# Kernel optimization log

Measured on AMD Instinct MI355X. Metric: run time of the kernel, lower is better.

## Reference

```python
import jax, jax.numpy as jnp
import numpy as np
import math

B, T, N, C = 1, 12, 10000, 32
TIME_DIM, N_SUP, E, NODE_EMB = 8, 3, 320000, 32
S = N_SUP + 2  # support_len + 2 slots after concat


def setup_inputs() -> dict:
    key = jax.random.key(0)
    ks = jax.random.split(key, 16)
    inp = {
        'x': jax.random.normal(ks[0], (B, T, N, C), jnp.float32),
        'timeoh': jax.random.uniform(ks[1], (B, 43), jnp.float32),
        'edges': jax.random.randint(ks[2], (N_SUP, 2, E), 0, N),
        # shared dy_gat params (attention_list reuses the same ModuleList)
        'mlp_w': jax.random.normal(ks[3], (C, C), jnp.float32) * 0.05,
        'mlp_b': jnp.zeros((C,), jnp.float32),
        'temb_w': jax.random.normal(ks[4], (43, TIME_DIM), jnp.float32) * 0.1,
        'atten_pool': jax.random.normal(ks[5], (TIME_DIM, 2 * C), jnp.float32) * 0.1,
        # adaptive-adjacency gcn branch
        'node2vec': jax.random.normal(ks[6], (N, NODE_EMB), jnp.float32) * 0.1,
        'gcn_w': jax.random.normal(ks[7], (3 * C, C), jnp.float32) * 0.05,
        'gcn_b': jnp.zeros((C,), jnp.float32),
        # slot self-attention over S supports
        'q_w': jax.random.normal(ks[8], (C, 6 * C), jnp.float32) * 0.05,
        'q_b': jnp.zeros((6 * C,), jnp.float32),
        'k_w': jax.random.normal(ks[9], (C, 6 * C), jnp.float32) * 0.05,
        'k_b': jnp.zeros((6 * C,), jnp.float32),
        'v_w': jax.random.normal(ks[10], (C, 6 * C), jnp.float32) * 0.05,
        'v_b': jnp.zeros((6 * C,), jnp.float32),
        'dense_w': jax.random.normal(ks[11], (6 * C, C), jnp.float32) * 0.05,
        'dense_b': jnp.zeros((C,), jnp.float32),
    }
    return inp


def _dy_gat(x, timeoh, src, dst, mlp_w, mlp_b, temb_w, atten_pool):
    h = x @ mlp_w + mlp_b                                   # (B,T,N,C)
    attn = (timeoh @ temb_w) @ atten_pool                    # (B,2C)
    # einsum('btnc,bc->btn') over concatenated [h_src, h_dst] splits additively
    s_src = jnp.einsum('btnc,bc->btn', h, attn[:, :C])
    s_dst = jnp.einsum('btnc,bc->btn', h, attn[:, C:])
    values = s_src[:, :, src] + s_dst[:, :, dst]             # (B,T,E)
    p = jax.nn.leaky_relu(values, 0.01)
    e = jnp.exp(p - jnp.max(p, axis=2, keepdims=True))       # global (per b,t) max-shift
    rowsum = jnp.zeros((B, T, N), e.dtype).at[:, :, src].add(e)
    h_prime = jnp.zeros_like(h).at[:, :, src].add(e[..., None] * h[:, :, dst, :])
    h_prime = h_prime / (rowsum[..., None] + 9e-15)
    return jax.nn.elu(h_prime)  # concat=True


def reference(x, timeoh, edges, mlp_w, mlp_b, temb_w, atten_pool,
              node2vec, gcn_w, gcn_b, q_w, q_b, k_w, k_b, v_w, v_b,
              dense_w, dense_b):
    outs = [x]
    for i in range(N_SUP):
        outs.append(_dy_gat(x, timeoh, edges[i, 0], edges[i, 1],
                            mlp_w, mlp_b, temb_w, atten_pool))
    # adaptive graph conv (static, order=2, support_len=1)
    adj = jax.nn.softmax(jax.nn.relu(node2vec @ node2vec.T), axis=1)  # (N,N)
    x1 = jnp.einsum('wv,btvf->btwf', adj, x)
    x2 = jnp.einsum('wv,btvf->btwf', adj, x1)
    x_adp = jnp.concatenate([x, x1, x2], -1) @ gcn_w + gcn_b
    outs.append(x_adp)
    out = jnp.concatenate(outs, -1).reshape(B, T, N, S, C)
    q = out @ q_w + q_b                                       # (B,T,N,S,6C)
    k = out @ k_w + k_b
    v = out @ v_w + v_b
    scores = jnp.einsum('btnsd,btnud->btnsu', q, k) / math.sqrt(6 * C)
    a = jax.nn.softmax(scores, axis=-1)
    o = jnp.einsum('btnsu,btnud->btnsd', a, v)
    o = o @ dense_w + dense_b                                 # (B,T,N,S,C)
    return jax.nn.elu(jnp.mean(o, axis=-2))                   # (B,T,N,C)
```

## Files before the change

### kernel.cpp

```cpp
#include <hip/hip_runtime.h>
#include <hip/hip_bf16.h>

#define T_ 12
#define N_ 10000
#define C_ 32
#define E_ 320000
#define SUP_ 3
#define TN_ (T_*N_)

typedef __attribute__((ext_vector_type(4))) float f32x4;
typedef __attribute__((ext_vector_type(8))) short bf16x8;
typedef __attribute__((ext_vector_type(4))) short bf16x4;

__device__ __forceinline__ short bf16c(float f) {
  __hip_bfloat16 b = __float2bfloat16(f);
  return (short)__builtin_bit_cast(unsigned short, b);
}

#if __has_builtin(__builtin_amdgcn_exp2f)
#define EXP2F(x) __builtin_amdgcn_exp2f(x)
#else
#define EXP2F(x) exp2f(x)
#endif

#define PRM_ATTN 0
#define PRM_G    64
#define PRM_H    1088
#define PRM_G1   2112
#define PRM_G2   2144
#define PRM_HB   2176
#define PRM_G0   2208

__global__ __launch_bounds__(256) void k_prep(
    const float* __restrict__ timeoh, const float* __restrict__ temb_w,
    const float* __restrict__ atten_pool,
    const float* __restrict__ q_w, const float* __restrict__ q_b,
    const float* __restrict__ k_w, const float* __restrict__ k_b,
    const float* __restrict__ v_w, const float* __restrict__ v_b,
    const float* __restrict__ dense_w, const float* __restrict__ dense_b,
    float* __restrict__ prm) {
  __shared__ float tv[8];
  int tid = threadIdx.x;
  if (tid < 8) {
    float s = 0.f;
    for (int j = 0; j < 43; j++) s += timeoh[j] * temb_w[j * 8 + tid];
    tv[tid] = s;
  }
  __syncthreads();
  if (tid < 64) {
    float s = 0.f;
    for (int d = 0; d < 8; d++) s += tv[d] * atten_pool[d * 64 + tid];
    prm[PRM_ATTN + tid] = s;
  }
  for (int idx = tid; idx < 1024; idx += 256) {
    int r = idx >> 5, c = idx & 31;
    float s = 0.f, s2 = 0.f;
    for (int d = 0; d < 192; d++) {
      s  += q_w[r * 192 + d] * k_w[c * 192 + d];
      s2 += v_w[r * 192 + d] * dense_w[d * 32 + c];
    }
    prm[PRM_G + idx] = s;
    prm[PRM_H + idx] = s2;
  }
  if (tid < 32) {
    float s = 0.f, s2 = 0.f, s3 = 0.f;
    for (int d = 0; d < 192; d++) {
      s  += q_w[tid * 192 + d] * k_b[d];
      s2 += k_w[tid * 192 + d] * q_b[d];
      s3 += v_b[d] * dense_w[d * 32 + tid];
    }
    prm[PRM_G1 + tid] = s;
    prm[PRM_G2 + tid] = s2;
    prm[PRM_HB + tid] = s3 + dense_b[tid];
  }
  if (tid == 0) {
    float s = 0.f;
    for (int d = 0; d < 192; d++) s += q_b[d] * k_b[d];
    prm[PRM_G0] = s;
  }
}

__global__ __launch_bounds__(256) void k_h(
    const float* __restrict__ x, const float* __restrict__ mlp_w,
    const float* __restrict__ mlp_b, const float* __restrict__ prm,
    __hip_bfloat16* __restrict__ h16, float* __restrict__ s_src,
    float* __restrict__ s_dst) {
  __shared__ float W[32 * 32];
  __shared__ float bsh[32], attnsh[64];
  __shared__ float xs[8][32];
  int tid = threadIdx.x;
  for (int i = tid; i < 1024; i += 256) W[i] = mlp_w[i];
  if (tid < 32) bsh[tid] = mlp_b[tid];
  if (tid < 64) attnsh[tid] = prm[PRM_ATTN + tid];
  long base = (long)blockIdx.x * 8;
  int nloc = tid >> 5, c = tid & 31;
  long row = base + nloc;
  xs[nloc][c] = x[row * 32 + c];
  __syncthreads();
  float hval = bsh[c];
#pragma unroll
  for (int k = 0; k < 32; k++) hval = fmaf(xs[nloc][k], W[k * 32 + c], hval);
  h16[row * 32 + c] = __float2bfloat16(hval);
  float a = hval * attnsh[c], b = hval * attnsh[32 + c];
#pragma unroll
  for (int m = 16; m >= 1; m >>= 1) {
    a += __shfl_xor(a, m, 64);
    b += __shfl_xor(b, m, 64);
  }
  if (c == 0) { s_src[row] = a; s_dst[row] = b; }
}

__global__ __launch_bounds__(256) void k_hist(const int* __restrict__ edges,
                                              int* __restrict__ cnt) {
  int sup = blockIdx.y;
  int e = blockIdx.x * 256 + threadIdx.x;
  const int* src = edges + (long)sup * 2 * E_;
  atomicAdd(&cnt[sup * N_ + src[e]], 1);
}

__global__ __launch_bounds__(1024) void k_scan(const int* __restrict__ cnt,
                                               int* __restrict__ offs,
                                               int* __restrict__ cur) {
  __shared__ int sh[1024];
  __shared__ int run;
  int sup = blockIdx.x, tid = threadIdx.x;
  if (tid == 0) run = 0;
  __syncthreads();
  for (int base = 0; base < N_; base += 1024) {
    int i = base + tid;
    int v = (i < N_) ? cnt[sup * N_ + i] : 0;
    sh[tid] = v;
    __syncthreads();
    for (int off = 1; off < 1024; off <<= 1) {
      int t = (tid >= off) ? sh[tid - off] : 0;
      __syncthreads();
      sh[tid] += t;
      __syncthreads();
    }
    int runv = run;
    int excl = runv + sh[tid] - v;
    if (i < N_) {
      offs[sup * (N_ + 1) + i] = excl;
      cur[sup * N_ + i] = excl;
    }
    __syncthreads();
    if (tid == 0) run = runv + sh[1023];
    __syncthreads();
  }
  if (tid == 0) offs[sup * (N_ + 1) + N_] = run;
}

__global__ __launch_bounds__(256) void k_fill(const int* __restrict__ edges,
                                              int* __restrict__ cur,
                                              int* __restrict__ csr) {
  int sup = blockIdx.y;
  int e = blockIdx.x * 256 + threadIdx.x;
  const int* src = edges + (long)sup * 2 * E_;
  const int* dst = src + E_;
  int pos = atomicAdd(&cur[sup * N_ + src[e]], 1);
  csr[sup * E_ + pos] = dst[e];
}

__global__ __launch_bounds__(256) void k_max(const int* __restrict__ edges,
                                             const float* __restrict__ s_src,
                                             const float* __restrict__ s_dst,
                                             unsigned* __restrict__ menc) {
  int sup = blockIdx.z, t = blockIdx.y;
  const int* src = edges + (long)sup * 2 * E_;
  const int* dst = src + E_;
  const float* ss = s_src + (long)t * N_;
  const float* sd = s_dst + (long)t * N_;
  float m = -1e30f;
  int lim = (blockIdx.x + 1) * 10000;
  for (int e = blockIdx.x * 10000 + threadIdx.x; e < lim; e += 256) {
    float v = ss[src[e]] + sd[dst[e]];
    v = (v >= 0.f) ? v : 0.01f * v;
    m = fmaxf(m, v);
  }
#pragma unroll
  for (int k = 32; k >= 1; k >>= 1) m = fmaxf(m, __shfl_xor(m, k, 64));
  if ((threadIdx.x & 63) == 0) {
    unsigned bits = __float_as_uint(m);
    unsigned enc = (bits & 0x80000000u) ? ~bits : (bits | 0x80000000u);
    atomicMax(&menc[sup * T_ + t], enc);
  }
}

__global__ __launch_bounds__(256) void k_gather(
    const int* __restrict__ csr, const int* __restrict__ offs,
    const float* __restrict__ s_src, const float* __restrict__ s_dst,
    const unsigned* __restrict__ menc, const __hip_bfloat16* __restrict__ h16,
    __hip_bfloat16* __restrict__ hp16) {
  const int sup = blockIdx.z, t = blockIdx.y;
  const int wave = threadIdx.x >> 6, lane = threadIdx.x & 63;
  const int n = blockIdx.x * 4 + wave;
  unsigned enc = menc[sup * T_ + t];
  unsigned mb = (enc & 0x80000000u) ? (enc & 0x7fffffffu) : ~enc;
  const float M = __uint_as_float(mb);
  const float a = s_src[(long)t * N_ + n];
  const int off = offs[sup * (N_ + 1) + n], end = offs[sup * (N_ + 1) + n + 1];
  const float* sd = s_dst + (long)t * N_;
  const uint4* hb4 = (const uint4*)(h16 + (long)t * N_ * 32);
  const int* csrs = csr + sup * E_;
  const int slot = lane >> 2, cl = lane & 3;
  const int clamp = (end > off) ? (end - 1) : 0;

  float acc[8];
#pragma unroll
  for (int j = 0; j < 8; j++) acc[j] = 0.f;
  float psum = 0.f;

  const int idx0 = off + slot;
  int d0 = csrs[min(idx0, clamp)];
  int d1 = csrs[min(idx0 + 16, clamp)];
  float sd0 = sd[d0];
  uint4 u0 = hb4[d0 * 4 + cl];

  for (int idx = idx0; idx < end; idx += 16) {
    int d2 = csrs[min(idx + 32, clamp)];
    float sd1 = sd[d1];
    uint4 u1 = hb4[d1 * 4 + cl];
    float v = a + sd0;
    v = fmaxf(v, 0.01f * v);
    float p = __expf(v - M);
    psum += p;
    acc[0] = fmaf(p, __uint_as_float(u0.x << 16),        acc[0]);
    acc[1] = fmaf(p, __uint_as_float(u0.x & 0xffff0000u), acc[1]);
    acc[2] = fmaf(p, __uint_as_float(u0.y << 16),        acc[2]);
    acc[3] = fmaf(p, __uint_as_float(u0.y & 0xffff0000u), acc[3]);
    acc[4] = fmaf(p, __uint_as_float(u0.z << 16),        acc[4]);
    acc[5] = fmaf(p, __uint_as_float(u0.z & 0xffff0000u), acc[5]);
    acc[6] = fmaf(p, __uint_as_float(u0.w << 16),        acc[6]);
    acc[7] = fmaf(p, __uint_as_float(u0.w & 0xffff0000u), acc[7]);
    d1 = d2; sd0 = sd1; u0 = u1;
  }

#pragma unroll
  for (int m = 4; m <= 32; m <<= 1) psum += __shfl_xor(psum, m, 64);
#pragma unroll
  for (int j = 0; j < 8; j++) {
#pragma unroll
    for (int m = 4; m <= 32; m <<= 1) acc[j] += __shfl_xor(acc[j], m, 64);
  }

  if (slot == 0) {
    float inv = 1.f / (psum + 9e-15f);
    unsigned w[4];
#pragma unroll
    for (int q = 0; q < 4; q++) {
      float h0 = acc[2 * q + 0] * inv;
      float h1 = acc[2 * q + 1] * inv;
      h0 = (h0 > 0.f) ? h0 : (__expf(h0) - 1.f);
      h1 = (h1 > 0.f) ? h1 : (__expf(h1) - 1.f);
      unsigned lo = (unsigned)(unsigned short)__builtin_bit_cast(unsigned short, __float2bfloat16(h0));
      unsigned hi = (unsigned)(unsigned short)__builtin_bit_cast(unsigned short, __float2bfloat16(h1));
      w[q] = lo | (hi << 16);
    }
    ((uint4*)hp16)[((long)sup * TN_ + (long)t * N_ + n) * 4 + cl] = uint4{w[0], w[1], w[2], w[3]};
  }
}

__global__ __launch_bounds__(256) void k_n2vA(const float* __restrict__ n2v,
                                              short* __restrict__ n2vA) {
  const float SC = 1.2011224087864498f;
  int idx = blockIdx.x * 256 + threadIdx.x;
  if (idx >= N_ * 4) return;
  int row = idx >> 2, l4 = idx & 3;
  short v[8];
#pragma unroll
  for (int h = 0; h < 2; h++)
#pragma unroll
    for (int j = 0; j < 4; j++)
      v[h * 4 + j] = bf16c(n2v[row * 32 + 16 * h + 4 * l4 + j] * SC);
  *(bf16x8*)&n2vA[(long)idx * 8] = bf16x8{v[0], v[1], v[2], v[3], v[4], v[5], v[6], v[7]};
}

template <int WITHR>
__global__ __launch_bounds__(256) void k_pack(const float* __restrict__ src,
                                              const float* __restrict__ rinv,
                                              short* __restrict__ xq) {
  int idx = blockIdx.x * 256 + threadIdx.x;
  int ck = idx / 1536;
  int rem = idx - ck * 1536;
  int l4 = rem / 384;
  int col = rem - l4 * 384;
  int t = col >> 5, f = col & 31;
  const long cb = (long)t * N_ * 32 + f;
  short v[8];
#pragma unroll
  for (int e = 0; e < 8; e++) {
    int vv = ck * 32 + 4 * l4 + (e & 3) + 16 * (e >> 2);
    float a = 0.f;
    if (vv < N_) {
      a = src[cb + (long)vv * 32];
      if (WITHR) a *= rinv[vv];
    }
    v[e] = bf16c(a);
  }
  *(bf16x8*)&xq[(long)idx * 8] = bf16x8{v[0], v[1], v[2], v[3], v[4], v[5], v[6], v[7]};
}

template <int PASS>
__global__ __launch_bounds__(512, 2) void k_adj12(const short* __restrict__ n2vA,
                                                  const short* __restrict__ xq,
                                                  float* __restrict__ out,
                                                  float* __restrict__ Rout) {
  __shared__ __align__(16) short aPl[2][8 * 4 * 64 * 8];
  const int tid = threadIdx.x;
  const int lane = tid & 63;
  const int wv = tid >> 6;
  const int l15 = lane & 15;
  const int l4 = lane >> 4;
  const int brow0 = blockIdx.x * 64;
  const int colbase = wv * 48;

  bf16x8 bw[4];
#pragma unroll
  for (int mt = 0; mt < 4; mt++) {
    int row = brow0 + mt * 16 + l15;
    row = row < N_ ? row : N_ - 1;
    bw[mt] = *(const bf16x8*)&n2vA[((long)row * 4 + l4) * 8];
  }

  f32x4 acc[4][3];
#pragma unroll
  for (int i = 0; i < 4; i++)
#pragma unroll
    for (int j = 0; j < 3; j++) acc[i][j] = f32x4{0.f, 0.f, 0.f, 0.f};
  float racc[4] = {0.f, 0.f, 0.f, 0.f};

#define PHASE_A(cexpr, slab)                                                              \
  {                                                                                       \
    const int c_ = (cexpr);                                                               \
    if (c_ < 313) {                                                                       \
      const int vb_ = c_ * 32;                                                            \
      int r1_ = vb_ + 16 + l15; r1_ = r1_ < N_ ? r1_ : N_ - 1;                            \
      bf16x8 av0_ = *(const bf16x8*)&n2vA[((long)(vb_ + l15) * 4 + l4) * 8];              \
      bf16x8 av1_ = *(const bf16x8*)&n2vA[((long)r1_ * 4 + l4) * 8];                      \
      _Pragma("unroll")                                                                   \
      for (int mt = 0; mt < 4; mt++) {                                                    \
        f32x4 s0_ = __builtin_amdgcn_mfma_f32_16x16x32_bf16(av0_, bw[mt],                 \
                                                            f32x4{0.f,0.f,0.f,0.f},0,0,0);\
        f32x4 s1_ = __builtin_amdgcn_mfma_f32_16x16x32_bf16(av1_, bw[mt],                 \
                                                            f32x4{0.f,0.f,0.f,0.f},0,0,0);\
        short pp_[8];                                                                     \
        float rs0_ = 0.f, rs1_ = 0.f;                                                     \
        _Pragma("unroll")                                                                 \
        for (int j = 0; j < 4; j++) {                                                     \
          float p0_ = EXP2F(fmaxf(s0_[j], 0.f));                                          \
          float p1_ = EXP2F(fmaxf(s1_[j], 0.f));                                          \
          if constexpr (PASS == 1) { rs0_ += p0_; rs1_ += p1_; }                          \
          pp_[j] = bf16c(p0_);                                                            \
          pp_[j + 4] = bf16c(p1_);                                                        \
        }                                                                                 \
        *(bf16x8*)&aPl[slab][((wv * 4 + mt) * 64 + lane) * 8] =                           \
            bf16x8{pp_[0],pp_[1],pp_[2],pp_[3],pp_[4],pp_[5],pp_[6],pp_[7]};              \
        if constexpr (PASS == 1) racc[mt] += (c_ != 312) ? (rs0_ + rs1_) : rs0_;          \
      }                                                                                   \
    }                                                                                     \
  }

  PHASE_A(wv, 0)
  __syncthreads();

  for (int g = 0; g < 40; g++) {
    const int cur = g & 1;
    if (g + 1 < 40) PHASE_A((g + 1) * 8 + wv, cur ^ 1)

    const int rem = 313 - g * 8;
    if (rem >= 8) {
      bf16x8 bx[24];
#pragma unroll
      for (int cc = 0; cc < 8; cc++) {
        const long xb = (long)(g * 8 + cc) * 1536 + (long)l4 * 384;
        bx[cc * 3 + 0] = *(const bf16x8*)&xq[(xb + colbase + 0 * 16 + l15) * 8];
        bx[cc * 3 + 1] = *(const bf16x8*)&xq[(xb + colbase + 1 * 16 + l15) * 8];
        bx[cc * 3 + 2] = *(const bf16x8*)&xq[(xb + colbase + 2 * 16 + l15) * 8];
      }
#pragma unroll
      for (int cc = 0; cc < 8; cc++) {
#pragma unroll
        for (int mt = 0; mt < 4; mt++) {
          bf16x8 aP = *(const bf16x8*)&aPl[cur][((cc * 4 + mt) * 64 + lane) * 8];
          acc[mt][0] = __builtin_amdgcn_mfma_f32_16x16x32_bf16(aP, bx[cc * 3 + 0], acc[mt][0], 0, 0, 0);
          acc[mt][1] = __builtin_amdgcn_mfma_f32_16x16x32_bf16(aP, bx[cc * 3 + 1], acc[mt][1], 0, 0, 0);
          acc[mt][2] = __builtin_amdgcn_mfma_f32_16x16x32_bf16(aP, bx[cc * 3 + 2], acc[mt][2], 0, 0, 0);
        }
      }
    } else {
      for (int cc = 0; cc < rem; cc++) {
        const long xb = (long)(g * 8 + cc) * 1536 + (long)l4 * 384;
        bf16x8 bx0 = *(const bf16x8*)&xq[(xb + colbase + 0 * 16 + l15) * 8];
        bf16x8 bx1 = *(const bf16x8*)&xq[(xb + colbase + 1 * 16 + l15) * 8];
        bf16x8 bx2 = *(const bf16x8*)&xq[(xb + colbase + 2 * 16 + l15) * 8];
#pragma unroll
        for (int mt = 0; mt < 4; mt++) {
          bf16x8 aP = *(const bf16x8*)&aPl[cur][((cc * 4 + mt) * 64 + lane) * 8];
          acc[mt][0] = __builtin_amdgcn_mfma_f32_16x16x32_bf16(aP, bx0, acc[mt][0], 0, 0, 0);
          acc[mt][1] = __builtin_amdgcn_mfma_f32_16x16x32_bf16(aP, bx1, acc[mt][1], 0, 0, 0);
          acc[mt][2] = __builtin_amdgcn_mfma_f32_16x16x32_bf16(aP, bx2, acc[mt][2], 0, 0, 0);
        }
      }
    }
    __syncthreads();
  }
#undef PHASE_A

  if constexpr (PASS == 1) {
#pragma unroll
    for (int mt = 0; mt < 4; mt++) {
      float r = racc[mt];
      r += __shfl_xor(r, 16, 64);
      r += __shfl_xor(r, 32, 64);
      int w = brow0 + mt * 16 + l15;
      if (l4 == 0 && w < N_) atomicAdd(&Rout[w], r);
    }
  }
#pragma unroll
  for (int mt = 0; mt < 4; mt++) {
#pragma unroll
    for (int nt = 0; nt < 3; nt++) {
      const int col = colbase + nt * 16 + l15;
      const int t = col >> 5, f = col & 31;
#pragma unroll
      for (int j = 0; j < 4; j++) {
        const int w = brow0 + mt * 16 + 4 * l4 + j;
        if (w < N_) out[((long)t * N_ + w) * 32 + f] = acc[mt][nt][j];
      }
    }
  }
}

__global__ __launch_bounds__(256) void k_rinv(float* __restrict__ R) {
  int i = blockIdx.x * 256 + threadIdx.x;
  if (i < N_) R[i] = 1.f / R[i];
}

__global__ __launch_bounds__(256) void k_gcn(const float* __restrict__ x,
                                             const float* __restrict__ x1,
                                             float* __restrict__ x2io,
                                             const float* __restrict__ Rinv,
                                             const float* __restrict__ gcn_w,
                                             const float* __restrict__ gcn_b) {
  __shared__ float W[96 * 32];
  __shared__ float bsh[32];
  __shared__ float rows[8][96];
  int tid = threadIdx.x;
  for (int i = tid; i < 96 * 32; i += 256) W[i] = gcn_w[i];
  if (tid < 32) bsh[tid] = gcn_b[tid];
  long base = (long)blockIdx.x * 8;
  int nloc = tid >> 5, c = tid & 31;
  long row = base + nloc;
  long nIdx = row % N_;
  float ri = Rinv[nIdx];
  rows[nloc][c] = x[row * 32 + c];
  rows[nloc][32 + c] = x1[row * 32 + c] * ri;
  rows[nloc][64 + c] = x2io[row * 32 + c] * ri;
  __syncthreads();
  float o = bsh[c];
#pragma unroll
  for (int k = 0; k < 96; k++) o = fmaf(rows[nloc][k], W[k * 32 + c], o);
  __syncthreads();
  x2io[row * 32 + c] = o;
}

__device__ __forceinline__ void load_row(int s, long r, const float* __restrict__ x,
                                         const __hip_bfloat16* __restrict__ hp16,
                                         const float* __restrict__ xadp, float* m) {
  if (s == 0 || s == 4) {
    const float4* p = (const float4*)((s == 0 ? x : xadp) + r * 32);
#pragma unroll
    for (int q = 0; q < 8; q++) {
      float4 v = p[q];
      m[q * 4 + 0] = v.x; m[q * 4 + 1] = v.y; m[q * 4 + 2] = v.z; m[q * 4 + 3] = v.w;
    }
  } else {
    const uint4* p = (const uint4*)(hp16 + ((long)(s - 1) * TN_ + r) * 32);
#pragma unroll
    for (int q = 0; q < 4; q++) {
      uint4 v = p[q];
      unsigned uu[4] = {v.x, v.y, v.z, v.w};
#pragma unroll
      for (int j = 0; j < 4; j++) {
        m[q * 8 + j * 2 + 0] = __uint_as_float(uu[j] << 16);
        m[q * 8 + j * 2 + 1] = __uint_as_float(uu[j] & 0xffff0000u);
      }
    }
  }
}

__global__ __launch_bounds__(256) void k_attn(const float* __restrict__ x,
                                              const __hip_bfloat16* __restrict__ hp16,
                                              const float* __restrict__ xadp,
                                              const float* __restrict__ prm,
                                              float* __restrict__ out) {
  __shared__ float Gs[1024], Hs[1024], g1s[32], g2s[32], hbs[32];
  __shared__ float g0sh;
  int tid = threadIdx.x;
  for (int i = tid; i < 1024; i += 256) { Gs[i] = prm[PRM_G + i]; Hs[i] = prm[PRM_H + i]; }
  if (tid < 32) { g1s[tid] = prm[PRM_G1 + tid]; g2s[tid] = prm[PRM_G2 + tid]; hbs[tid] = prm[PRM_HB + tid]; }
  if (tid == 0) g0sh = prm[PRM_G0];
  __syncthreads();
  long r = (long)blockIdx.x * 256 + tid;
  if (r >= TN_) return;
  float g0 = g0sh;
  float sc[5][5], d1[5], d2[5];
  float ms[32], mu[32], y[32];
#pragma unroll
  for (int s = 0; s < 5; s++) {
    load_row(s, r, x, hp16, xadp, ms);
    float a = 0.f, b = 0.f;
#pragma unroll
    for (int k = 0; k < 32; k++) { a = fmaf(ms[k], g1s[k], a); b = fmaf(ms[k], g2s[k], b); }
    d1[s] = a; d2[s] = b;
#pragma unroll
    for (int c = 0; c < 32; c++) {
      float s2 = 0.f;
#pragma unroll
      for (int k = 0; k < 32; k++) s2 = fmaf(ms[k], Gs[k * 32 + c], s2);
      y[c] = s2;
    }
#pragma unroll
    for (int u = 0; u < 5; u++) {
      load_row(u, r, x, hp16, xadp, mu);
      float dt = 0.f;
#pragma unroll
      for (int k = 0; k < 32; k++) dt = fmaf(y[k], mu[k], dt);
      sc[s][u] = dt;
    }
  }
  const float rs = 0.07216878364870322f;
  float abar[5];
#pragma unroll
  for (int u = 0; u < 5; u++) abar[u] = 0.f;
#pragma unroll
  for (int s = 0; s < 5; s++) {
    float e[5];
    float mx = -1e30f;
#pragma unroll
    for (int u = 0; u < 5; u++) {
      float v = (sc[s][u] + d1[s] + d2[u] + g0) * rs;
      e[u] = v;
      mx = fmaxf(mx, v);
    }
    float sm = 0.f;
#pragma unroll
    for (int u = 0; u < 5; u++) { e[u] = __expf(e[u] - mx); sm += e[u]; }
    float inv = 1.f / sm;
#pragma unroll
    for (int u = 0; u < 5; u++) abar[u] = fmaf(e[u], inv, abar[u]);
  }
  float z[32];
#pragma unroll
  for (int k = 0; k < 32; k++) z[k] = 0.f;
#pragma unroll
  for (int u = 0; u < 5; u++) {
    load_row(u, r, x, hp16, xadp, mu);
    float w = abar[u] * 0.2f;
#pragma unroll
    for (int k = 0; k < 32; k++) z[k] = fmaf(w, mu[k], z[k]);
  }
#pragma unroll
  for (int c = 0; c < 32; c++) {
    float o = hbs[c];
#pragma unroll
    for (int k = 0; k < 32; k++) o = fmaf(z[k], Hs[k * 32 + c], o);
    o = (o > 0.f) ? o : (__expf(o) - 1.f);
    out[r * 32 + c] = o;
  }
}

extern "C" void kernel_launch(void* const* d_in, const int* in_sizes, int n_in,
                              void* d_out, int out_size, void* d_ws, size_t ws_size,
                              hipStream_t stream) {
  (void)in_sizes; (void)n_in; (void)out_size; (void)ws_size;
  const float* x          = (const float*)d_in[0];
  const float* timeoh     = (const float*)d_in[1];
  const int*   edges      = (const int*)d_in[2];
  const float* mlp_w      = (const float*)d_in[3];
  const float* mlp_b      = (const float*)d_in[4];
  const float* temb_w     = (const float*)d_in[5];
  const float* atten_pool = (const float*)d_in[6];
  const float* node2vec   = (const float*)d_in[7];
  const float* gcn_w      = (const float*)d_in[8];
  const float* gcn_b      = (const float*)d_in[9];
  const float* q_w  = (const float*)d_in[10];
  const float* q_b  = (const float*)d_in[11];
  const float* k_w  = (const float*)d_in[12];
  const float* k_b  = (const float*)d_in[13];
  const float* v_w  = (const float*)d_in[14];
  const float* v_b  = (const float*)d_in[15];
  const float* dense_w = (const float*)d_in[16];
  const float* dense_b = (const float*)d_in[17];
  float* out = (float*)d_out;
  char* ws = (char*)d_ws;

  float*    prm  = (float*)(ws + 0);
  unsigned* menc = (unsigned*)(ws + 9216);
  int*      cnt  = (int*)(ws + 9472);
  int*      cur  = (int*)(ws + 129472);
  int*      offs = (int*)(ws + 249472);
  float*    ssrc = (float*)(ws + 369664);
  float*    sdst = (float*)(ws + 849664);
  float*    R    = (float*)(ws + 1329664);
  __hip_bfloat16* h16  = (__hip_bfloat16*)(ws + 1369664);
  int*      csr  = (int*)(ws + 9049664);
  __hip_bfloat16* hp16 = (__hip_bfloat16*)(ws + 12889664);
  float*    x1   = (float*)(ws + 35929664);
  float*    x2   = (float*)(ws + 51289664);
  short*    n2vA = (short*)(ws + 66649664);
  short*    xq0  = (short*)(ws + 67289664);
  short*    xq1  = (short*)(ws + 74983488);

  (void)hipMemsetAsync(menc, 0, 144, stream);
  (void)hipMemsetAsync(cnt, 0, 120000, stream);
  (void)hipMemsetAsync(R, 0, 40000, stream);

  k_prep<<<1, 256, 0, stream>>>(timeoh, temb_w, atten_pool, q_w, q_b, k_w, k_b,
                                v_w, v_b, dense_w, dense_b, prm);
  k_h<<<15000, 256, 0, stream>>>(x, mlp_w, mlp_b, prm, h16, ssrc, sdst);
  k_hist<<<dim3(1250, 3), 256, 0, stream>>>(edges, cnt);
  k_scan<<<3, 1024, 0, stream>>>(cnt, offs, cur);
  k_fill<<<dim3(1250, 3), 256, 0, stream>>>(edges, cur, csr);
  k_max<<<dim3(32, 12, 3), 256, 0, stream>>>(edges, ssrc, sdst, menc);
  k_gather<<<dim3(2500, 12, 3), 256, 0, stream>>>(csr, offs, ssrc, sdst, menc, h16, hp16);

  k_n2vA<<<157, 256, 0, stream>>>(node2vec, n2vA);
  k_pack<0><<<1878, 256, 0, stream>>>(x, nullptr, xq0);
  k_adj12<1><<<157, 512, 0, stream>>>(n2vA, xq0, x1, R);
  k_rinv<<<40, 256, 0, stream>>>(R);
  k_pack<1><<<1878, 256, 0, stream>>>(x1, R, xq1);
  k_adj12<2><<<157, 512, 0, stream>>>(n2vA, xq1, x2, nullptr);
  k_gcn<<<15000, 256, 0, stream>>>(x, x1, x2, R, gcn_w, gcn_b);
  k_attn<<<469, 256, 0, stream>>>(x, hp16, x2, prm, out);
}
```

Measured before the change: 923.8 us.

## Retile adjacency GEMM to 128 rows by 192 columns per block

The fused adjacency-softmax-times-x kernel now gives each block 128 output rows and half of the 384 columns, on a 79x2 grid instead of 157 blocks. The 8 waves split both the exp(score) tile generation (two row halves by four column chunks) and the MFMA accumulation (two row groups by four column groups). Each block now produces a larger probability tile per stage and reuses it across more rows, so less score recomputation happens per output. In exchange, the exp work is duplicated across the two column-half blocks, and the row-sum atomics are restricted to blockIdx.y==0.

```diff
diff --git a/kernel.cpp b/kernel.cpp
--- a/kernel.cpp
+++ b/kernel.cpp
@@ -301,23 +301,27 @@
 }
 
 template <int PASS>
-__global__ __launch_bounds__(512, 2) void k_adj12(const short* __restrict__ n2vA,
+__global__ __launch_bounds__(512, 2) void k_adj13(const short* __restrict__ n2vA,
                                                   const short* __restrict__ xq,
                                                   float* __restrict__ out,
                                                   float* __restrict__ Rout) {
-  __shared__ __align__(16) short aPl[2][8 * 4 * 64 * 8];
+  __shared__ __align__(16) short aPl[2][4 * 8 * 64 * 8];
   const int tid = threadIdx.x;
   const int lane = tid & 63;
   const int wv = tid >> 6;
   const int l15 = lane & 15;
   const int l4 = lane >> 4;
-  const int brow0 = blockIdx.x * 64;
-  const int colbase = wv * 48;
+  const int brow0 = blockIdx.x * 128;
+  const int mh = wv & 1;
+  const int cslot = wv >> 1;
+  const int mgrp = wv >> 2;
+  const int cgw = wv & 3;
+  const int colg = blockIdx.y * 192 + cgw * 48;
 
   bf16x8 bw[4];
 #pragma unroll
   for (int mt = 0; mt < 4; mt++) {
-    int row = brow0 + mt * 16 + l15;
+    int row = brow0 + (mh * 4 + mt) * 16 + l15;
     row = row < N_ ? row : N_ - 1;
     bw[mt] = *(const bf16x8*)&n2vA[((long)row * 4 + l4) * 8];
   }
@@ -329,11 +333,11 @@
     for (int j = 0; j < 3; j++) acc[i][j] = f32x4{0.f, 0.f, 0.f, 0.f};
   float racc[4] = {0.f, 0.f, 0.f, 0.f};
 
-#define PHASE_A(cexpr, slab)                                                              \
+#define PHASE_A(gexpr, slab)                                                              \
   {                                                                                       \
-    const int c_ = (cexpr);                                                               \
-    if (c_ < 313) {                                                                       \
-      const int vb_ = c_ * 32;                                                            \
+    const int co_ = (gexpr) * 4 + cslot;                                                  \
+    if (co_ < 313) {                                                                      \
+      const int vb_ = co_ * 32;                                                           \
       int r1_ = vb_ + 16 + l15; r1_ = r1_ < N_ ? r1_ : N_ - 1;                            \
       bf16x8 av0_ = *(const bf16x8*)&n2vA[((long)(vb_ + l15) * 4 + l4) * 8];              \
       bf16x8 av1_ = *(const bf16x8*)&n2vA[((long)r1_ * 4 + l4) * 8];                      \
@@ -353,49 +357,50 @@
           pp_[j] = bf16c(p0_);                                                            \
           pp_[j + 4] = bf16c(p1_);                                                        \
         }                                                                                 \
-        *(bf16x8*)&aPl[slab][((wv * 4 + mt) * 64 + lane) * 8] =                           \
+        *(bf16x8*)&aPl[slab][((cslot * 8 + mh * 4 + mt) * 64 + lane) * 8] =               \
             bf16x8{pp_[0],pp_[1],pp_[2],pp_[3],pp_[4],pp_[5],pp_[6],pp_[7]};              \
-        if constexpr (PASS == 1) racc[mt] += (c_ != 312) ? (rs0_ + rs1_) : rs0_;          \
+        if constexpr (PASS == 1) racc[mt] += (co_ != 312) ? (rs0_ + rs1_) : rs0_;         \
       }                                                                                   \
     }                                                                                     \
   }
 
-  PHASE_A(wv, 0)
+  PHASE_A(0, 0)
   __syncthreads();
 
-  for (int g = 0; g < 40; g++) {
+  const int NGRP = 79;
+  for (int g = 0; g < NGRP; g++) {
     const int cur = g & 1;
-    if (g + 1 < 40) PHASE_A((g + 1) * 8 + wv, cur ^ 1)
-
-    const int rem = 313 - g * 8;
-    if (rem >= 8) {
-      bf16x8 bx[24];
-#pragma unroll
-      for (int cc = 0; cc < 8; cc++) {
-        const long xb = (long)(g * 8 + cc) * 1536 + (long)l4 * 384;
-        bx[cc * 3 + 0] = *(const bf16x8*)&xq[(xb + colbase + 0 * 16 + l15) * 8];
-        bx[cc * 3 + 1] = *(const bf16x8*)&xq[(xb + colbase + 1 * 16 + l15) * 8];
-        bx[cc * 3 + 2] = *(const bf16x8*)&xq[(xb + colbase + 2 * 16 + l15) * 8];
+    if (g + 1 < NGRP) PHASE_A(g + 1, cur ^ 1)
+
+    const int rem0 = 313 - g * 4;
+    if (rem0 >= 4) {
+      bf16x8 bx[12];
+#pragma unroll
+      for (int cc = 0; cc < 4; cc++) {
+        const long xb = (long)(g * 4 + cc) * 1536 + (long)l4 * 384;
+        bx[cc * 3 + 0] = *(const bf16x8*)&xq[(xb + colg + 0 * 16 + l15) * 8];
+        bx[cc * 3 + 1] = *(const bf16x8*)&xq[(xb + colg + 1 * 16 + l15) * 8];
+        bx[cc * 3 + 2] = *(const bf16x8*)&xq[(xb + colg + 2 * 16 + l15) * 8];
       }
 #pragma unroll
-      for (int cc = 0; cc < 8; cc++) {
+      for (int cc = 0; cc < 4; cc++) {
 #pragma unroll
         for (int mt = 0; mt < 4; mt++) {
-          bf16x8 aP = *(const bf16x8*)&aPl[cur][((cc * 4 + mt) * 64 + lane) * 8];
+          bf16x8 aP = *(const bf16x8*)&aPl[cur][((cc * 8 + mgrp * 4 + mt) * 64 + lane) * 8];
           acc[mt][0] = __builtin_amdgcn_mfma_f32_16x16x32_bf16(aP, bx[cc * 3 + 0], acc[mt][0], 0, 0, 0);
           acc[mt][1] = __builtin_amdgcn_mfma_f32_16x16x32_bf16(aP, bx[cc * 3 + 1], acc[mt][1], 0, 0, 0);
           acc[mt][2] = __builtin_amdgcn_mfma_f32_16x16x32_bf16(aP, bx[cc * 3 + 2], acc[mt][2], 0, 0, 0);
         }
       }
     } else {
-      for (int cc = 0; cc < rem; cc++) {
-        const long xb = (long)(g * 8 + cc) * 1536 + (long)l4 * 384;
-        bf16x8 bx0 = *(const bf16x8*)&xq[(xb + colbase + 0 * 16 + l15) * 8];
-        bf16x8 bx1 = *(const bf16x8*)&xq[(xb + colbase + 1 * 16 + l15) * 8];
-        bf16x8 bx2 = *(const bf16x8*)&xq[(xb + colbase + 2 * 16 + l15) * 8];
+      for (int cc = 0; cc < rem0; cc++) {
+        const long xb = (long)(g * 4 + cc) * 1536 + (long)l4 * 384;
+        bf16x8 bx0 = *(const bf16x8*)&xq[(xb + colg + 0 * 16 + l15) * 8];
+        bf16x8 bx1 = *(const bf16x8*)&xq[(xb + colg + 1 * 16 + l15) * 8];
+        bf16x8 bx2 = *(const bf16x8*)&xq[(xb + colg + 2 * 16 + l15) * 8];
 #pragma unroll
         for (int mt = 0; mt < 4; mt++) {
-          bf16x8 aP = *(const bf16x8*)&aPl[cur][((cc * 4 + mt) * 64 + lane) * 8];
+          bf16x8 aP = *(const bf16x8*)&aPl[cur][((cc * 8 + mgrp * 4 + mt) * 64 + lane) * 8];
           acc[mt][0] = __builtin_amdgcn_mfma_f32_16x16x32_bf16(aP, bx0, acc[mt][0], 0, 0, 0);
           acc[mt][1] = __builtin_amdgcn_mfma_f32_16x16x32_bf16(aP, bx1, acc[mt][1], 0, 0, 0);
           acc[mt][2] = __builtin_amdgcn_mfma_f32_16x16x32_bf16(aP, bx2, acc[mt][2], 0, 0, 0);
@@ -407,24 +412,26 @@
 #undef PHASE_A
 
   if constexpr (PASS == 1) {
-#pragma unroll
-    for (int mt = 0; mt < 4; mt++) {
-      float r = racc[mt];
-      r += __shfl_xor(r, 16, 64);
-      r += __shfl_xor(r, 32, 64);
-      int w = brow0 + mt * 16 + l15;
-      if (l4 == 0 && w < N_) atomicAdd(&Rout[w], r);
+    if (blockIdx.y == 0) {
+#pragma unroll
+      for (int mt = 0; mt < 4; mt++) {
+        float r = racc[mt];
+        r += __shfl_xor(r, 16, 64);
+        r += __shfl_xor(r, 32, 64);
+        int w = brow0 + (mh * 4 + mt) * 16 + l15;
+        if (l4 == 0 && w < N_) atomicAdd(&Rout[w], r);
+      }
     }
   }
 #pragma unroll
   for (int mt = 0; mt < 4; mt++) {
 #pragma unroll
     for (int nt = 0; nt < 3; nt++) {
-      const int col = colbase + nt * 16 + l15;
+      const int col = colg + nt * 16 + l15;
       const int t = col >> 5, f = col & 31;
 #pragma unroll
       for (int j = 0; j < 4; j++) {
-        const int w = brow0 + mt * 16 + 4 * l4 + j;
+        const int w = brow0 + mgrp * 64 + mt * 16 + 4 * l4 + j;
         if (w < N_) out[((long)t * N_ + w) * 32 + f] = acc[mt][nt][j];
       }
     }
@@ -627,10 +634,10 @@
 
   k_n2vA<<<157, 256, 0, stream>>>(node2vec, n2vA);
   k_pack<0><<<1878, 256, 0, stream>>>(x, nullptr, xq0);
-  k_adj12<1><<<157, 512, 0, stream>>>(n2vA, xq0, x1, R);
+  k_adj13<1><<<dim3(79, 2), 512, 0, stream>>>(n2vA, xq0, x1, R);
   k_rinv<<<40, 256, 0, stream>>>(R);
   k_pack<1><<<1878, 256, 0, stream>>>(x1, R, xq1);
-  k_adj12<2><<<157, 512, 0, stream>>>(n2vA, xq1, x2, nullptr);
+  k_adj13<2><<<dim3(79, 2), 512, 0, stream>>>(n2vA, xq1, x2, nullptr);
   k_gcn<<<15000, 256, 0, stream>>>(x, x1, x2, R, gcn_w, gcn_b);
   k_attn<<<469, 256, 0, stream>>>(x, hp16, x2, prm, out);
 }
```

Result: slower. 1.007 ms (+9.0%).
